# Performance work log

Measured on AMD Instinct MI355X. Metric: run time of the kernel, lower is better.

Reference implementation:

```python
import jax, jax.numpy as jnp
import numpy as np

NC = 80          # classes
REG_MAX = 16     # DFL bins
NK = 51          # 17*3 keypoint channels
KPT_SHAPE = (17, 3)
MAX_DET = 100
CONF_THRES = 0.25
STRIDES = (8, 16, 32)


def _conv1x1(f, w, b):
    # f: (B,C,H,W), w: (O,C), b: (O,) -> (B,O,H,W)
    return jnp.einsum('bchw,oc->bohw', f, w) + b[None, :, None, None]


def _make_anchors(shapes, strides, offset=0.5):
    pts, sts = [], []
    for (h, w), s in zip(shapes, strides):
        sx = jnp.arange(w, dtype=jnp.float32) + offset
        sy = jnp.arange(h, dtype=jnp.float32) + offset
        gy, gx = jnp.meshgrid(sy, sx, indexing='ij')
        pts.append(jnp.stack([gx, gy], -1).reshape(-1, 2))
        sts.append(jnp.full((h * w, 1), float(s), jnp.float32))
    # transposed as in _new_inference: anchors (2,A), strides (1,A)
    return jnp.concatenate(pts, 0).T, jnp.concatenate(sts, 0).T


def setup_inputs() -> dict:
    key = jax.random.key(0)
    ks = jax.random.split(key, 16)
    ch = (128, 256, 512)
    hw = ((80, 80), (40, 40), (20, 20))
    d = {}
    for i, (c, (h, w)) in enumerate(zip(ch, hw)):
        d[f'x{i}'] = jax.random.normal(ks[i], (16, c, h, w), jnp.float32)
    k = 3
    for name, oc in (('cv2', 4 * REG_MAX), ('cv3', NC), ('cv4', NK)):
        for i, c in enumerate(ch):
            d[f'{name}_w{i}'] = jax.random.normal(ks[k], (oc, c), jnp.float32) * 0.02
            d[f'{name}_b{i}'] = jnp.zeros((oc,), jnp.float32)
            k += 1
    return d


def reference(x0, x1, x2,
              cv2_w0, cv2_b0, cv2_w1, cv2_b1, cv2_w2, cv2_b2,
              cv3_w0, cv3_b0, cv3_w1, cv3_b1, cv3_w2, cv3_b2,
              cv4_w0, cv4_b0, cv4_w1, cv4_b1, cv4_w2, cv4_b2):
    feats = [x0, x1, x2]
    cv2 = [(cv2_w0, cv2_b0), (cv2_w1, cv2_b1), (cv2_w2, cv2_b2)]
    cv3 = [(cv3_w0, cv3_b0), (cv3_w1, cv3_b1), (cv3_w2, cv3_b2)]
    cv4 = [(cv4_w0, cv4_b0), (cv4_w1, cv4_b1), (cv4_w2, cv4_b2)]
    bs = x0.shape[0]

    # keypoint branch: cat over levels -> (bs, nk, A)
    kpt = jnp.concatenate(
        [_conv1x1(f, w, b).reshape(bs, NK, -1) for f, (w, b) in zip(feats, cv4)], -1)
    # box+cls branch -> (bs, 4*reg_max+nc, A)
    xcat = jnp.concatenate(
        [jnp.concatenate([_conv1x1(f, *cv2[i]), _conv1x1(f, *cv3[i])], 1).reshape(bs, 4 * REG_MAX + NC, -1)
         for i, f in enumerate(feats)], -1)
    box, cls = xcat[:, :4 * REG_MAX], xcat[:, 4 * REG_MAX:]

    shapes = [(f.shape[2], f.shape[3]) for f in feats]
    anchors, strides = _make_anchors(shapes, STRIDES)  # (2,A), (1,A)
    A = anchors.shape[1]

    # DFL decode: softmax over reg_max bins, expectation w/ arange weights
    p = jax.nn.softmax(box.reshape(bs, 4, REG_MAX, A), axis=2)
    dist = jnp.einsum('bfra,r->bfa', p, jnp.arange(REG_MAX, dtype=jnp.float32))
    lt, rb = dist[:, :2], dist[:, 2:]
    x1y1 = anchors[None] - lt
    x2y2 = anchors[None] + rb
    # xywh box coding, scaled by strides
    dbox = jnp.concatenate([(x1y1 + x2y2) * 0.5, x2y2 - x1y1], 1) * strides[None]  # (bs,4,A)

    # keypoint decode (Pose.kpts_decode, ndim==3)
    y = kpt.reshape(bs, KPT_SHAPE[0], KPT_SHAPE[1], A)
    kxy = (y[:, :, :2] * 2.0 + (anchors[None, None] - 0.5)) * strides[None, None]
    kv = jax.nn.sigmoid(y[:, :, 2:3])
    pred_kpts = jnp.concatenate([kxy, kv], 2).reshape(bs, NK, A).transpose(0, 2, 1)  # (bs,A,nk)

    # EfficientIdxNMS_TRT stand-in: sigmoid scores (score_activation=1),
    # class-agnostic deterministic top-k selection by best class score.
    scores = jax.nn.sigmoid(cls.transpose(0, 2, 1))  # (bs,A,nc)
    max_s = scores.max(-1)
    cls_id = jnp.argmax(scores, -1)
    top_s, top_i = jax.lax.top_k(max_s, MAX_DET)     # (bs,MAX_DET)
    num_dets = (top_s > CONF_THRES).sum(-1).astype(jnp.int32)[:, None]
    det_boxes = jnp.take_along_axis(dbox.transpose(0, 2, 1), top_i[..., None], 1)  # (bs,MAX_DET,4)
    det_classes = jnp.take_along_axis(cls_id, top_i, 1).astype(jnp.int32)
    # irregular keypoint gather via det indices (the pred_kpts[bs_indices, det_indices] step)
    det_kpts = jnp.take_along_axis(pred_kpts, top_i[..., None], 1).reshape(bs, MAX_DET, *KPT_SHAPE)
    return num_dets, det_boxes, top_s, det_classes, det_kpts
```

## Files before the change

kernel.cpp:

```cpp
#include <hip/hip_runtime.h>
#include <hip/hip_bf16.h>

#define NC 80
#define NK 51
#define REG_MAX 16
#define MAX_DET 100
#define A_TOT 8400
#define BS 16

#define OUT_NUM 0
#define OUT_BOX 16
#define OUT_SCORE (16 + 16*MAX_DET*4)
#define OUT_CLASS (OUT_SCORE + 16*MAX_DET)
#define OUT_KPT (OUT_CLASS + 16*MAX_DET)

static __device__ __forceinline__ unsigned long long mk_key(unsigned u, int a) {
    return ((unsigned long long)u << 32) | (unsigned)(0x7FFFFFFF - a);
}

__global__ __launch_bounds__(256) void scores_fused(
    const float* __restrict__ x0, const float* __restrict__ x1, const float* __restrict__ x2,
    const float* __restrict__ w0, const float* __restrict__ w1, const float* __restrict__ w2,
    const float* __restrict__ bias0, const float* __restrict__ bias1, const float* __restrict__ bias2,
    float* __restrict__ max_s,
    int* __restrict__ cls_id)
{
    __shared__ float fs[32 * 128];
    __shared__ float wsh[80 * 32];
    __shared__ float rm[4][128];
    __shared__ int   ri[4][128];

    int bid = blockIdx.x;
    const float *x, *w, *bias; int C, A, a_off, b, tile;
    if (bid < 64) {
        x = x2; w = w2; bias = bias2; C = 512; A = 400; a_off = 8000;
        b = bid >> 2; tile = bid & 3;
    } else if (bid < 272) {
        int r = bid - 64;
        x = x1; w = w1; bias = bias1; C = 256; A = 1600; a_off = 6400;
        b = r / 13; tile = r - b * 13;
    } else {
        int r = bid - 272;
        x = x0; w = w0; bias = bias0; C = 128; A = 6400; a_off = 0;
        b = r / 50; tile = r - b * 50;
    }
    int a0 = tile * 128;

    int t = threadIdx.x;
    int lane = t & 63;
    int wv = t >> 6;
    int oc0 = wv * 20;

    float acc0[20], acc1[20];
#pragma unroll
    for (int j = 0; j < 20; ++j) { float bv = bias[oc0 + j]; acc0[j] = bv; acc1[j] = bv; }

    const float* xb = x + (long)b * C * A;
    int nchunk = C >> 5;

    for (int kc = 0; kc < nchunk; ++kc) {
        __syncthreads();
#pragma unroll
        for (int i = 0; i < 4; ++i) {
            int idx = t + i * 256;
            int c = idx >> 5;
            int q = (idx & 31) * 4;
            int aa = a0 + q; if (aa > A - 4) aa = A - 4;
            float4 v = *(const float4*)(xb + (long)(kc * 32 + c) * A + aa);
            *(float4*)(&fs[c * 128 + q]) = v;
        }
#pragma unroll
        for (int i = 0; i < 3; ++i) {
            int idx = t + i * 256;
            if (idx < 640) {
                int oc = idx >> 3;
                int q = (idx & 7) * 4;
                float4 v = *(const float4*)(w + oc * C + kc * 32 + q);
                *(float4*)(&wsh[oc * 32 + q]) = v;
            }
        }
        __syncthreads();

#pragma unroll 1
        for (int c4 = 0; c4 < 32; c4 += 4) {
            float fa[4], fb[4];
#pragma unroll
            for (int cc = 0; cc < 4; ++cc) {
                fa[cc] = fs[(c4 + cc) * 128 + lane];
                fb[cc] = fs[(c4 + cc) * 128 + lane + 64];
            }
#pragma unroll
            for (int j = 0; j < 20; ++j) {
                float4 w4 = *(const float4*)(&wsh[(oc0 + j) * 32 + c4]);
                acc0[j] = fmaf(w4.x, fa[0], acc0[j]);
                acc0[j] = fmaf(w4.y, fa[1], acc0[j]);
                acc0[j] = fmaf(w4.z, fa[2], acc0[j]);
                acc0[j] = fmaf(w4.w, fa[3], acc0[j]);
                acc1[j] = fmaf(w4.x, fb[0], acc1[j]);
                acc1[j] = fmaf(w4.y, fb[1], acc1[j]);
                acc1[j] = fmaf(w4.z, fb[2], acc1[j]);
                acc1[j] = fmaf(w4.w, fb[3], acc1[j]);
            }
        }
    }

    float m0 = acc0[0], m1 = acc1[0]; int i0 = 0, i1 = 0;
#pragma unroll
    for (int j = 1; j < 20; ++j) {
        if (acc0[j] > m0) { m0 = acc0[j]; i0 = j; }
        if (acc1[j] > m1) { m1 = acc1[j]; i1 = j; }
    }
    i0 += oc0; i1 += oc0;

    rm[wv][lane] = m0;      ri[wv][lane] = i0;
    rm[wv][lane + 64] = m1; ri[wv][lane + 64] = i1;
    __syncthreads();
    if (wv == 0) {
#pragma unroll
        for (int p = 0; p < 2; ++p) {
            int a = lane + p * 64;
            float bm = rm[0][a]; int bi = ri[0][a];
#pragma unroll
            for (int v = 1; v < 4; ++v) {
                float om = rm[v][a];
                if (om > bm) { bm = om; bi = ri[v][a]; }
            }
            int ga = a0 + a;
            if (ga < A) {
                max_s[b * A_TOT + a_off + ga] = 1.0f / (1.0f + expf(-bm));
                cls_id[b * A_TOT + a_off + ga] = bi;
            }
        }
    }
}

__global__ __launch_bounds__(1024) void topk_kernel(
    const float* __restrict__ max_s,
    const int* __restrict__ cls_id,
    float* __restrict__ out,
    int* __restrict__ top_idx)
{
    int b = blockIdx.x;
    int t = threadIdx.x;
    int wv = t >> 6;

    __shared__ unsigned hist[16 * 256];
    __shared__ unsigned suffix[256];
    __shared__ int tieIdx[A_TOT];
    __shared__ unsigned long long highKeys[128];
    __shared__ unsigned long long finalKeys[128];
    __shared__ int wmin[16];
    __shared__ unsigned s_prefix;
    __shared__ int s_k, s_selD, s_nHigh, s_nTie, s_cnt, s_bcast;

    unsigned u[9];
    bool val[9];
#pragma unroll
    for (int i = 0; i < 9; ++i) {
        int a = t + i * 1024;
        val[i] = (a < A_TOT);
        u[i] = val[i] ? __float_as_uint(max_s[b * A_TOT + a]) : 0u;
    }

    if (t == 0) { s_prefix = 0; s_k = MAX_DET; s_nHigh = 0; s_nTie = 0; s_cnt = 0; }

    for (int pass = 0; pass < 4; ++pass) {
#pragma unroll
        for (int j = 0; j < 4; ++j) hist[t + j * 1024] = 0;
        if (t == 0) s_selD = 0;
        __syncthreads();

        unsigned pre = s_prefix;
        int k = s_k;
        int shHi = 32 - 8 * pass;
        int shD = 24 - 8 * pass;
#pragma unroll
        for (int i = 0; i < 9; ++i) {
            if (val[i]) {
                bool cand = (pass == 0) ? true : ((u[i] >> shHi) == pre);
                if (cand)
                    atomicAdd(&hist[(wv << 8) + ((u[i] >> shD) & 0xFF)], 1u);
            }
        }
        __syncthreads();

        if (t < 256) {
            unsigned s = 0;
#pragma unroll
            for (int w = 0; w < 16; ++w) s += hist[(w << 8) + t];
            suffix[t] = s;
        }
        __syncthreads();
        for (int off = 1; off < 256; off <<= 1) {
            unsigned v = 0;
            if (t < 256) v = suffix[t] + ((t + off < 256) ? suffix[t + off] : 0u);
            __syncthreads();
            if (t < 256) suffix[t] = v;
            __syncthreads();
        }
        if (t < 256 && suffix[t] >= (unsigned)k) atomicMax(&s_selD, t);
        __syncthreads();
        if (t == 0) {
            int d = s_selD;
            s_k = k - ((d < 255) ? (int)suffix[d + 1] : 0);
            s_prefix = (pre << 8) | (unsigned)d;
        }
        __syncthreads();
    }

    unsigned cut = s_prefix;
    int r = s_k;

#pragma unroll
    for (int i = 0; i < 9; ++i) {
        if (val[i]) {
            int a = t + i * 1024;
            if (u[i] > cut) {
                int p = atomicAdd(&s_nHigh, 1);
                highKeys[p] = mk_key(u[i], a);
            } else if (u[i] == cut) {
                int p = atomicAdd(&s_nTie, 1);
                tieIdx[p] = a;
            }
        }
    }
    __syncthreads();
    int m = s_nHigh;
    int nt = s_nTie;

    if (t < 128) finalKeys[t] = 0ull;
    __syncthreads();
    if (t < m) finalKeys[t] = highKeys[t];

    if (nt == r) {
        if (t < nt) finalKeys[m + t] = mk_key(cut, tieIdx[t]);
        __syncthreads();
    } else {
        __syncthreads();
        for (int j = 0; j < r; ++j) {
            int mn = 0x7FFFFFFF;
            for (int p = t; p < nt; p += 1024) mn = min(mn, tieIdx[p]);
            for (int off = 32; off > 0; off >>= 1) mn = min(mn, __shfl_down(mn, off, 64));
            if ((t & 63) == 0) wmin[wv] = mn;
            __syncthreads();
            if (t == 0) {
                int v = wmin[0];
#pragma unroll
                for (int w = 1; w < 16; ++w) v = min(v, wmin[w]);
                s_bcast = v;
                finalKeys[m + j] = mk_key(cut, v);
            }
            __syncthreads();
            int v = s_bcast;
            for (int p = t; p < nt; p += 1024)
                if (tieIdx[p] == v) tieIdx[p] = 0x7FFFFFFF;
            __syncthreads();
        }
    }

    for (int ksz = 2; ksz <= 128; ksz <<= 1) {
        for (int j = ksz >> 1; j > 0; j >>= 1) {
            if (t < 128) {
                int ixj = t ^ j;
                if (ixj > t) {
                    bool desc = ((t & ksz) == 0);
                    unsigned long long x = finalKeys[t], y = finalKeys[ixj];
                    bool sw = desc ? (x < y) : (x > y);
                    if (sw) { finalKeys[t] = y; finalKeys[ixj] = x; }
                }
            }
            __syncthreads();
        }
    }

    if (t < MAX_DET) {
        unsigned long long kk = finalKeys[t];
        float sc = __uint_as_float((unsigned)(kk >> 32));
        int a = 0x7FFFFFFF - (int)(kk & 0xFFFFFFFFull);
        out[OUT_SCORE + b * MAX_DET + t] = sc;
        out[OUT_CLASS + b * MAX_DET + t] = (float)cls_id[b * A_TOT + a];
        top_idx[b * MAX_DET + t] = a;
        if (sc > 0.25f) atomicAdd(&s_cnt, 1);
    }
    __syncthreads();
    if (t == 0) out[OUT_NUM + b] = (float)s_cnt;
}

__global__ __launch_bounds__(128) void decode_kernel(
    const float* __restrict__ x0, const float* __restrict__ x1, const float* __restrict__ x2,
    const float* __restrict__ w2_0, const float* __restrict__ b2_0,
    const float* __restrict__ w2_1, const float* __restrict__ b2_1,
    const float* __restrict__ w2_2, const float* __restrict__ b2_2,
    const float* __restrict__ w4_0, const float* __restrict__ b4_0,
    const float* __restrict__ w4_1, const float* __restrict__ b4_1,
    const float* __restrict__ w4_2, const float* __restrict__ b4_2,
    const int* __restrict__ top_idx,
    float* __restrict__ out)
{
    int b = blockIdx.y;
    int k = blockIdx.x;
    int a = top_idx[b * MAX_DET + k];

    const float* x; const float* w2; const float* bb2; const float* w4; const float* bb4;
    int C, A, W, a_local; float stride;
    if (a < 6400)      { x = x0; C = 128; A = 6400; W = 80; stride = 8.0f;  a_local = a;        w2 = w2_0; bb2 = b2_0; w4 = w4_0; bb4 = b4_0; }
    else if (a < 8000) { x = x1; C = 256; A = 1600; W = 40; stride = 16.0f; a_local = a - 6400; w2 = w2_1; bb2 = b2_1; w4 = w4_1; bb4 = b4_1; }
    else               { x = x2; C = 512; A = 400;  W = 20; stride = 32.0f; a_local = a - 8000; w2 = w2_2; bb2 = b2_2; w4 = w4_2; bb4 = b4_2; }

    __shared__ float fs[512];
    __shared__ float logits[64];
    __shared__ float kraw[NK];
    __shared__ float dist[4];

    int t = threadIdx.x;
    for (int c = t; c < C; c += 128)
        fs[c] = x[((long)b * C + c) * A + a_local];
    __syncthreads();

    if (t < 64 + NK) {
        const float* wrow; float acc;
        if (t < 64) { wrow = w2 + t * C; acc = bb2[t]; }
        else        { wrow = w4 + (t - 64) * C; acc = bb4[t - 64]; }
        for (int c = 0; c < C; ++c) acc = fmaf(wrow[c], fs[c], acc);
        if (t < 64) logits[t] = acc;
        else        kraw[t - 64] = acc;
    }
    __syncthreads();

    if (t < 4) {
        float mx = logits[t * 16];
#pragma unroll
        for (int r = 1; r < 16; ++r) mx = fmaxf(mx, logits[t * 16 + r]);
        float se = 0.0f, sw = 0.0f;
#pragma unroll
        for (int r = 0; r < 16; ++r) {
            float e = expf(logits[t * 16 + r] - mx);
            se += e; sw += e * (float)r;
        }
        dist[t] = sw / se;
    }
    __syncthreads();

    float ax = (float)(a_local % W) + 0.5f;
    float ay = (float)(a_local / W) + 0.5f;

    if (t == 0) {
        float x1c = ax - dist[0], y1c = ay - dist[1];
        float x2c = ax + dist[2], y2c = ay + dist[3];
        float* ob = out + OUT_BOX + ((long)b * MAX_DET + k) * 4;
        ob[0] = (x1c + x2c) * 0.5f * stride;
        ob[1] = (y1c + y2c) * 0.5f * stride;
        ob[2] = (x2c - x1c) * stride;
        ob[3] = (y2c - y1c) * stride;
    }
    if (t < 17) {
        float vx = kraw[t * 3], vy = kraw[t * 3 + 1], vv = kraw[t * 3 + 2];
        float gx = ax - 0.5f, gy = ay - 0.5f;
        float* ok = out + OUT_KPT + (((long)b * MAX_DET + k) * 17 + t) * 3;
        ok[0] = (vx * 2.0f + gx) * stride;
        ok[1] = (vy * 2.0f + gy) * stride;
        ok[2] = 1.0f / (1.0f + expf(-vv));
    }
}

extern "C" void kernel_launch(void* const* d_in, const int* in_sizes, int n_in,
                              void* d_out, int out_size, void* d_ws, size_t ws_size,
                              hipStream_t stream) {
    const float* x0 = (const float*)d_in[0];
    const float* x1 = (const float*)d_in[1];
    const float* x2 = (const float*)d_in[2];
    const float* w2[3] = {(const float*)d_in[3], (const float*)d_in[5], (const float*)d_in[7]};
    const float* b2[3] = {(const float*)d_in[4], (const float*)d_in[6], (const float*)d_in[8]};
    const float* w3[3] = {(const float*)d_in[9], (const float*)d_in[11], (const float*)d_in[13]};
    const float* b3[3] = {(const float*)d_in[10], (const float*)d_in[12], (const float*)d_in[14]};
    const float* w4[3] = {(const float*)d_in[15], (const float*)d_in[17], (const float*)d_in[19]};
    const float* b4[3] = {(const float*)d_in[16], (const float*)d_in[18], (const float*)d_in[20]};

    float* out = (float*)d_out;

    float* ws_maxs = (float*)d_ws;
    int* ws_cls = (int*)(ws_maxs + BS * A_TOT);
    int* ws_top = (int*)(ws_cls + BS * A_TOT);

    scores_fused<<<dim3(1072), 256, 0, stream>>>(
        x0, x1, x2, w3[0], w3[1], w3[2], b3[0], b3[1], b3[2], ws_maxs, ws_cls);
    topk_kernel<<<dim3(BS), 1024, 0, stream>>>(ws_maxs, ws_cls, out, ws_top);
    decode_kernel<<<dim3(MAX_DET, BS), 128, 0, stream>>>(
        x0, x1, x2,
        w2[0], b2[0], w2[1], b2[1], w2[2], b2[2],
        w4[0], b4[0], w4[1], b4[1], w4[2], b4[2],
        ws_top, out);
}
```

Before: 302.2 us.

## Restructure class-score GEMM: 256-anchor tiles, register prefetch, weights read directly

The class-score 1x1-conv kernel now uses 512-thread blocks over 256-anchor tiles. Each lane computes 4 adjacent anchors for 10 output channels, instead of 2 anchors for 20 channels. Features are prefetched into registers one chunk ahead, which removes one barrier per chunk and overlaps global loads with compute. Weights are read straight from global memory as wave-uniform loads instead of being staged in shared memory. The aim is fewer blocks, better LDS vectorisation and latency hiding, at the cost of higher register pressure and an 8-wave argmax reduction at the end.

```diff
diff --git a/kernel.cpp b/kernel.cpp
--- a/kernel.cpp
+++ b/kernel.cpp
@@ -18,118 +18,129 @@
     return ((unsigned long long)u << 32) | (unsigned)(0x7FFFFFFF - a);
 }
 
-__global__ __launch_bounds__(256) void scores_fused(
+__global__ __launch_bounds__(512, 4) void scores_fused(
     const float* __restrict__ x0, const float* __restrict__ x1, const float* __restrict__ x2,
     const float* __restrict__ w0, const float* __restrict__ w1, const float* __restrict__ w2,
     const float* __restrict__ bias0, const float* __restrict__ bias1, const float* __restrict__ bias2,
     float* __restrict__ max_s,
     int* __restrict__ cls_id)
 {
-    __shared__ float fs[32 * 128];
-    __shared__ float wsh[80 * 32];
-    __shared__ float rm[4][128];
-    __shared__ int   ri[4][128];
+    __shared__ float fs[32 * 256];
 
     int bid = blockIdx.x;
     const float *x, *w, *bias; int C, A, a_off, b, tile;
-    if (bid < 64) {
+    if (bid < 32) {
         x = x2; w = w2; bias = bias2; C = 512; A = 400; a_off = 8000;
-        b = bid >> 2; tile = bid & 3;
-    } else if (bid < 272) {
-        int r = bid - 64;
+        b = bid >> 1; tile = bid & 1;
+    } else if (bid < 144) {
+        int r = bid - 32;
         x = x1; w = w1; bias = bias1; C = 256; A = 1600; a_off = 6400;
-        b = r / 13; tile = r - b * 13;
+        b = r / 7; tile = r - b * 7;
     } else {
-        int r = bid - 272;
+        int r = bid - 144;
         x = x0; w = w0; bias = bias0; C = 128; A = 6400; a_off = 0;
-        b = r / 50; tile = r - b * 50;
-    }
-    int a0 = tile * 128;
+        b = r / 25; tile = r - b * 25;
+    }
+    int a0 = tile * 256;
 
     int t = threadIdx.x;
     int lane = t & 63;
-    int wv = t >> 6;
-    int oc0 = wv * 20;
-
-    float acc0[20], acc1[20];
-#pragma unroll
-    for (int j = 0; j < 20; ++j) { float bv = bias[oc0 + j]; acc0[j] = bv; acc1[j] = bv; }
+    int lane4 = lane * 4;
+    int wv = __builtin_amdgcn_readfirstlane(t >> 6);
+    int oc0 = wv * 10;
+
+    float acc[10][4];
+#pragma unroll
+    for (int j = 0; j < 10; ++j) {
+        float bv = bias[oc0 + j];
+#pragma unroll
+        for (int an = 0; an < 4; ++an) acc[j][an] = bv;
+    }
 
     const float* xb = x + (long)b * C * A;
     int nchunk = C >> 5;
 
+    float4 r[4];
+#pragma unroll
+    for (int i = 0; i < 4; ++i) {
+        int idx = t + i * 512;
+        int c = idx >> 6;
+        int aa = a0 + ((idx & 63) << 2);
+        if (aa > A - 4) aa = A - 4;
+        r[i] = *(const float4*)(xb + (long)c * A + aa);
+    }
+
     for (int kc = 0; kc < nchunk; ++kc) {
-        __syncthreads();
-#pragma unroll
-        for (int i = 0; i < 4; ++i) {
-            int idx = t + i * 256;
-            int c = idx >> 5;
-            int q = (idx & 31) * 4;
-            int aa = a0 + q; if (aa > A - 4) aa = A - 4;
-            float4 v = *(const float4*)(xb + (long)(kc * 32 + c) * A + aa);
-            *(float4*)(&fs[c * 128 + q]) = v;
-        }
-#pragma unroll
-        for (int i = 0; i < 3; ++i) {
-            int idx = t + i * 256;
-            if (idx < 640) {
-                int oc = idx >> 3;
-                int q = (idx & 7) * 4;
-                float4 v = *(const float4*)(w + oc * C + kc * 32 + q);
-                *(float4*)(&wsh[oc * 32 + q]) = v;
-            }
-        }
-        __syncthreads();
-
+#pragma unroll
+        for (int i = 0; i < 4; ++i)
+            *(float4*)&fs[(t + i * 512) * 4] = r[i];
+        if (kc + 1 < nchunk) {
+#pragma unroll
+            for (int i = 0; i < 4; ++i) {
+                int idx = t + i * 512;
+                int c = (kc + 1) * 32 + (idx >> 6);
+                int aa = a0 + ((idx & 63) << 2);
+                if (aa > A - 4) aa = A - 4;
+                r[i] = *(const float4*)(xb + (long)c * A + aa);
+            }
+        }
+        __syncthreads();
+
+        const float* wbase = w + oc0 * C + kc * 32;
 #pragma unroll 1
         for (int c4 = 0; c4 < 32; c4 += 4) {
-            float fa[4], fb[4];
-#pragma unroll
-            for (int cc = 0; cc < 4; ++cc) {
-                fa[cc] = fs[(c4 + cc) * 128 + lane];
-                fb[cc] = fs[(c4 + cc) * 128 + lane + 64];
-            }
-#pragma unroll
-            for (int j = 0; j < 20; ++j) {
-                float4 w4 = *(const float4*)(&wsh[(oc0 + j) * 32 + c4]);
-                acc0[j] = fmaf(w4.x, fa[0], acc0[j]);
-                acc0[j] = fmaf(w4.y, fa[1], acc0[j]);
-                acc0[j] = fmaf(w4.z, fa[2], acc0[j]);
-                acc0[j] = fmaf(w4.w, fa[3], acc0[j]);
-                acc1[j] = fmaf(w4.x, fb[0], acc1[j]);
-                acc1[j] = fmaf(w4.y, fb[1], acc1[j]);
-                acc1[j] = fmaf(w4.z, fb[2], acc1[j]);
-                acc1[j] = fmaf(w4.w, fb[3], acc1[j]);
-            }
-        }
-    }
-
-    float m0 = acc0[0], m1 = acc1[0]; int i0 = 0, i1 = 0;
-#pragma unroll
-    for (int j = 1; j < 20; ++j) {
-        if (acc0[j] > m0) { m0 = acc0[j]; i0 = j; }
-        if (acc1[j] > m1) { m1 = acc1[j]; i1 = j; }
-    }
-    i0 += oc0; i1 += oc0;
-
-    rm[wv][lane] = m0;      ri[wv][lane] = i0;
-    rm[wv][lane + 64] = m1; ri[wv][lane + 64] = i1;
-    __syncthreads();
-    if (wv == 0) {
-#pragma unroll
-        for (int p = 0; p < 2; ++p) {
-            int a = lane + p * 64;
-            float bm = rm[0][a]; int bi = ri[0][a];
-#pragma unroll
-            for (int v = 1; v < 4; ++v) {
-                float om = rm[v][a];
-                if (om > bm) { bm = om; bi = ri[v][a]; }
-            }
-            int ga = a0 + a;
-            if (ga < A) {
-                max_s[b * A_TOT + a_off + ga] = 1.0f / (1.0f + expf(-bm));
-                cls_id[b * A_TOT + a_off + ga] = bi;
-            }
+            float4 f0 = *(const float4*)&fs[(c4 + 0) * 256 + lane4];
+            float4 f1 = *(const float4*)&fs[(c4 + 1) * 256 + lane4];
+            float4 f2 = *(const float4*)&fs[(c4 + 2) * 256 + lane4];
+            float4 f3 = *(const float4*)&fs[(c4 + 3) * 256 + lane4];
+#pragma unroll
+            for (int j = 0; j < 10; ++j) {
+                float4 wj = *(const float4*)(wbase + j * C + c4);
+                acc[j][0] = fmaf(wj.x, f0.x, acc[j][0]);
+                acc[j][0] = fmaf(wj.y, f1.x, acc[j][0]);
+                acc[j][0] = fmaf(wj.z, f2.x, acc[j][0]);
+                acc[j][0] = fmaf(wj.w, f3.x, acc[j][0]);
+                acc[j][1] = fmaf(wj.x, f0.y, acc[j][1]);
+                acc[j][1] = fmaf(wj.y, f1.y, acc[j][1]);
+                acc[j][1] = fmaf(wj.z, f2.y, acc[j][1]);
+                acc[j][1] = fmaf(wj.w, f3.y, acc[j][1]);
+                acc[j][2] = fmaf(wj.x, f0.z, acc[j][2]);
+                acc[j][2] = fmaf(wj.y, f1.z, acc[j][2]);
+                acc[j][2] = fmaf(wj.z, f2.z, acc[j][2]);
+                acc[j][2] = fmaf(wj.w, f3.z, acc[j][2]);
+                acc[j][3] = fmaf(wj.x, f0.w, acc[j][3]);
+                acc[j][3] = fmaf(wj.y, f1.w, acc[j][3]);
+                acc[j][3] = fmaf(wj.z, f2.w, acc[j][3]);
+                acc[j][3] = fmaf(wj.w, f3.w, acc[j][3]);
+            }
+        }
+        __syncthreads();
+    }
+
+    float* rm = fs;
+    int*   ri = (int*)(fs + 2048);
+#pragma unroll
+    for (int an = 0; an < 4; ++an) {
+        float m = acc[0][an]; int mi = 0;
+#pragma unroll
+        for (int j = 1; j < 10; ++j)
+            if (acc[j][an] > m) { m = acc[j][an]; mi = j; }
+        rm[wv * 256 + lane4 + an] = m;
+        ri[wv * 256 + lane4 + an] = mi + oc0;
+    }
+    __syncthreads();
+
+    if (t < 256) {
+        float bm = rm[t]; int bi = ri[t];
+#pragma unroll
+        for (int v = 1; v < 8; ++v) {
+            float om = rm[v * 256 + t];
+            if (om > bm) { bm = om; bi = ri[v * 256 + t]; }
+        }
+        int ga = a0 + t;
+        if (ga < A) {
+            max_s[b * A_TOT + a_off + ga] = 1.0f / (1.0f + expf(-bm));
+            cls_id[b * A_TOT + a_off + ga] = bi;
         }
     }
 }
@@ -382,7 +393,7 @@
     int* ws_cls = (int*)(ws_maxs + BS * A_TOT);
     int* ws_top = (int*)(ws_cls + BS * A_TOT);
 
-    scores_fused<<<dim3(1072), 256, 0, stream>>>(
+    scores_fused<<<dim3(544), 512, 0, stream>>>(
         x0, x1, x2, w3[0], w3[1], w3[2], b3[0], b3[1], b3[2], ws_maxs, ws_cls);
     topk_kernel<<<dim3(BS), 1024, 0, stream>>>(ws_maxs, ws_cls, out, ws_top);
     decode_kernel<<<dim3(MAX_DET, BS), 128, 0, stream>>>(
```

Measured after the change: 374.3 us. +23.8%, slower.
